# Performance work log

Hardware: AMD Instinct MI355X
Metric: run time of the kernel (lower is better)

Reference implementation:

```python
import jax, jax.numpy as jnp
import numpy as np

N_NODES = 100000
N_EDGES = 600000
IN_CH = 128
HID = 128


def setup_inputs() -> dict:
    key = jax.random.key(0)
    ks = jax.random.split(key, 8)
    x = jax.random.normal(ks[0], (N_NODES, IN_CH), dtype=jnp.float32)
    edge_index = jax.random.randint(ks[1], (2, N_EDGES), 0, N_NODES, dtype=jnp.int64)
    # Linear weights stored as (in, out); scaled like torch default init
    W1 = jax.random.normal(ks[2], (2 * IN_CH, HID), dtype=jnp.float32) / np.sqrt(2 * IN_CH)
    b1 = jnp.zeros((HID,), dtype=jnp.float32)
    W2 = jax.random.normal(ks[3], (HID, HID), dtype=jnp.float32) / np.sqrt(HID)
    b2 = jnp.zeros((HID,), dtype=jnp.float32)
    W3 = jax.random.normal(ks[4], (HID, 1), dtype=jnp.float32) / np.sqrt(HID)
    b3 = jnp.zeros((1,), dtype=jnp.float32)
    return {"x": x, "edge_index": edge_index, "W1": W1, "b1": b1,
            "W2": W2, "b2": b2, "W3": W3, "b3": b3}


def reference(x, edge_index, W1, b1, W2, b2, W3, b3):
    src = edge_index[0]
    tgt = edge_index[1]
    # gather + concat: [n_edges, 2*in_channels]
    h = jnp.concatenate([x[src, :], x[tgt, :]], axis=1)
    h = jax.nn.elu(h @ W1 + b1)
    h = jax.nn.elu(h @ W2 + b2)
    h = h @ W3 + b3  # [n_edges, 1]
    return jnp.squeeze(h)  # squeeze=True path -> [n_edges]
```

## Files before the change

kernel.cpp:

```cpp
#include <hip/hip_runtime.h>

#define N_NODES 100000
#define N_EDGES 600000
#define NT1 782
#define NT2 9375
#define LDH 136
#define G1H 512

typedef _Float16 f16x8 __attribute__((ext_vector_type(8)));
typedef __attribute__((ext_vector_type(4))) float f32x4;

__device__ __forceinline__ float elu_f(float v) {
    return v > 0.0f ? v : (__expf(v) - 1.0f);
}

extern "C" __global__ __launch_bounds__(256, 4)
void k1_node_linear(const float* __restrict__ x, const float* __restrict__ W1,
                    _Float16* __restrict__ P) {
    __shared__ __align__(16) _Float16 sX[128 * LDH];

    const int t = threadIdx.x;
    const int w = t >> 6, lane = t & 63;
    const int ln = lane & 15, kg = lane >> 4;
    const int kcf = t & 15;
    const int lef = t >> 4;
    const int half = (blockIdx.x >= G1H) ? 1 : 0;
    const int t0 = blockIdx.x - half * G1H;

    f16x8 bf[2][4];
#pragma unroll
    for (int c = 0; c < 2; ++c) {
        const int n = w * 32 + c * 16 + ln;
#pragma unroll
        for (int ks = 0; ks < 4; ++ks) {
            f16x8 v;
#pragma unroll
            for (int j = 0; j < 8; ++j) {
                int k = half * 128 + ks * 32 + kg * 8 + j;
                v[j] = (_Float16)W1[k * 128 + n];
            }
            bf[c][ks] = v;
        }
    }

    for (int tile = t0; tile < NT1; tile += G1H) {
        const int n0 = tile * 128;
        __syncthreads();
#pragma unroll 2
        for (int r = 0; r < 8; ++r) {
            int le = r * 16 + lef;
            int n = n0 + le;
            float4 a0 = make_float4(0.f, 0.f, 0.f, 0.f), a1 = a0;
            if (n < N_NODES) {
                const float* p = x + (size_t)n * 128 + kcf * 8;
                a0 = *(const float4*)p; a1 = *(const float4*)(p + 4);
            }
            float f[8] = {a0.x, a0.y, a0.z, a0.w, a1.x, a1.y, a1.z, a1.w};
            f16x8 vh;
#pragma unroll
            for (int j = 0; j < 8; ++j) vh[j] = (_Float16)f[j];
            *(f16x8*)(&sX[le * LDH + kcf * 8]) = vh;
        }
        __syncthreads();

        f32x4 acc[8][2];
#pragma unroll
        for (int rt = 0; rt < 8; ++rt)
#pragma unroll
            for (int c = 0; c < 2; ++c) acc[rt][c] = (f32x4){0.f, 0.f, 0.f, 0.f};

#pragma unroll
        for (int ks = 0; ks < 4; ++ks) {
#pragma unroll
            for (int rt = 0; rt < 8; ++rt) {
                f16x8 a = *(const f16x8*)(&sX[(rt * 16 + ln) * LDH + ks * 32 + kg * 8]);
#pragma unroll
                for (int c = 0; c < 2; ++c)
                    acc[rt][c] = __builtin_amdgcn_mfma_f32_16x16x32_f16(a, bf[c][ks], acc[rt][c], 0, 0, 0);
            }
        }

        __syncthreads();
#pragma unroll
        for (int rt = 0; rt < 8; ++rt)
#pragma unroll
            for (int c = 0; c < 2; ++c) {
                int col = w * 32 + c * 16 + ln;
#pragma unroll
                for (int reg = 0; reg < 4; ++reg) {
                    int row = rt * 16 + kg * 4 + reg;
                    sX[row * LDH + col] = (_Float16)acc[rt][c][reg];
                }
            }
        __syncthreads();
        {
            int row_l = t >> 1, seg = t & 1;
            int n = n0 + row_l;
            if (n < N_NODES) {
                _Float16* dst = P + (size_t)n * 256 + half * 128 + seg * 64;
                const _Float16* srcp = &sX[row_l * LDH + seg * 64];
#pragma unroll
                for (int i = 0; i < 8; ++i)
                    *(f16x8*)(dst + i * 8) = *(const f16x8*)(srcp + i * 8);
            }
        }
    }
}

extern "C" __global__ __launch_bounds__(256, 3)
void k2_edge_mlp(const _Float16* __restrict__ P, const void* __restrict__ eiv,
                 const float* __restrict__ b1, const float* __restrict__ W2,
                 const float* __restrict__ b2, const float* __restrict__ W3,
                 const float* __restrict__ b3, float* __restrict__ out) {
    __shared__ __align__(16) _Float16 sH[2][64 * LDH];
    __shared__ float sPart[2][4][64];
    __shared__ int sFlag;

    const int t = threadIdx.x;
    const int w = t >> 6, lane = t & 63;
    const int ln = lane & 15, kg = lane >> 4;
    const int row = t >> 2;
    const int kc0 = (t & 3) * 4;
    const float b3v = b3[0];
    const int stride = gridDim.x;

    if (t < 64) {
        unsigned v = ((const unsigned*)eiv)[2 * t + 1];
        unsigned long long bm = __ballot(v == 0u);
        if (t == 0) sFlag = (bm == ~0ull) ? 1 : 0;
    }

    f16x8 b1f[4];
#pragma unroll
    for (int i = 0; i < 4; ++i)
#pragma unroll
        for (int j = 0; j < 8; ++j) b1f[i][j] = (_Float16)b1[(kc0 + i) * 8 + j];

    float w3v[2], b2v[2];
#pragma unroll
    for (int c = 0; c < 2; ++c) {
        int col = w * 32 + c * 16 + ln;
        w3v[c] = W3[col]; b2v[c] = b2[col];
    }

    f16x8 bfw[2][4];
#pragma unroll
    for (int c = 0; c < 2; ++c) {
        const int n = w * 32 + c * 16 + ln;
#pragma unroll
        for (int ks = 0; ks < 4; ++ks) {
            f16x8 v;
#pragma unroll
            for (int j = 0; j < 8; ++j) {
                int k = ks * 32 + kg * 8 + j;
                v[j] = (_Float16)W2[k * 128 + n];
            }
            bfw[c][ks] = v;
        }
    }
    __syncthreads();
    const int mode64 = sFlag;

    const int tile0 = blockIdx.x;

    int se_nx, ge_nx;
    {
        int e = tile0 * 64 + row;
        if (mode64) {
            se_nx = (int)((const long long*)eiv)[e];
            ge_nx = (int)((const long long*)eiv)[N_EDGES + e];
        } else {
            se_nx = ((const int*)eiv)[e];
            ge_nx = ((const int*)eiv)[N_EDGES + e];
        }
    }
    {
        const _Float16* pa = P + (size_t)se_nx * 256 + kc0 * 8;
        const _Float16* pb = P + (size_t)ge_nx * 256 + 128 + kc0 * 8;
        f16x8 Ga[4], Gb[4];
#pragma unroll
        for (int i = 0; i < 4; ++i) {
            Ga[i] = *(const f16x8*)(pa + i * 8);
            Gb[i] = *(const f16x8*)(pb + i * 8);
        }
#pragma unroll
        for (int i = 0; i < 4; ++i) {
            f16x8 vh;
#pragma unroll
            for (int j = 0; j < 8; ++j)
                vh[j] = (_Float16)elu_f((float)Ga[i][j] + (float)Gb[i][j] + (float)b1f[i][j]);
            *(f16x8*)(&sH[0][row * LDH + (kc0 + i) * 8]) = vh;
        }
    }
    {
        int t1 = tile0 + stride;
        int t1c = (t1 < NT2) ? t1 : tile0;
        int e = t1c * 64 + row;
        if (mode64) {
            se_nx = (int)((const long long*)eiv)[e];
            ge_nx = (int)((const long long*)eiv)[N_EDGES + e];
        } else {
            se_nx = ((const int*)eiv)[e];
            ge_nx = ((const int*)eiv)[N_EDGES + e];
        }
    }
    __syncthreads();

    int p = 0;
    int prevE0 = -1;
    for (int tile = tile0; tile < NT2; tile += stride) {
        const int nt = tile + stride;
        const int ntc = (nt < NT2) ? nt : tile;

        const _Float16* pa = P + (size_t)se_nx * 256 + kc0 * 8;
        const _Float16* pb = P + (size_t)ge_nx * 256 + 128 + kc0 * 8;
        f16x8 Ga[4], Gb[4];
#pragma unroll
        for (int i = 0; i < 4; ++i) {
            Ga[i] = *(const f16x8*)(pa + i * 8);
            Gb[i] = *(const f16x8*)(pb + i * 8);
        }

        {
            int n2 = nt + stride;
            int n2c = (n2 < NT2) ? n2 : ntc;
            int e = n2c * 64 + row;
            if (mode64) {
                se_nx = (int)((const long long*)eiv)[e];
                ge_nx = (int)((const long long*)eiv)[N_EDGES + e];
            } else {
                se_nx = ((const int*)eiv)[e];
                ge_nx = ((const int*)eiv)[N_EDGES + e];
            }
        }

        if (prevE0 >= 0 && t < 64)
            out[prevE0 + t] = sPart[p ^ 1][0][t] + sPart[p ^ 1][1][t] +
                              sPart[p ^ 1][2][t] + sPart[p ^ 1][3][t] + b3v;

        f32x4 acc[4][2];
#pragma unroll
        for (int rt = 0; rt < 4; ++rt)
#pragma unroll
            for (int c = 0; c < 2; ++c) acc[rt][c] = (f32x4){0.f, 0.f, 0.f, 0.f};

#pragma unroll
        for (int ks = 0; ks < 4; ++ks) {
#pragma unroll
            for (int rt = 0; rt < 4; ++rt) {
                f16x8 a = *(const f16x8*)(&sH[p][(rt * 16 + ln) * LDH + ks * 32 + kg * 8]);
#pragma unroll
                for (int c = 0; c < 2; ++c)
                    acc[rt][c] = __builtin_amdgcn_mfma_f32_16x16x32_f16(a, bfw[c][ks], acc[rt][c], 0, 0, 0);
            }
        }

#pragma unroll
        for (int rt = 0; rt < 4; ++rt) {
            float pr[4] = {0.f, 0.f, 0.f, 0.f};
#pragma unroll
            for (int c = 0; c < 2; ++c) {
#pragma unroll
                for (int reg = 0; reg < 4; ++reg)
                    pr[reg] += elu_f(acc[rt][c][reg] + b2v[c]) * w3v[c];
            }
#pragma unroll
            for (int m = 1; m < 16; m <<= 1)
#pragma unroll
                for (int reg = 0; reg < 4; ++reg) pr[reg] += __shfl_xor(pr[reg], m, 64);
            if (ln == 0) {
#pragma unroll
                for (int reg = 0; reg < 4; ++reg)
                    sPart[p][w][rt * 16 + kg * 4 + reg] = pr[reg];
            }
        }

#pragma unroll
        for (int i = 0; i < 4; ++i) {
            f16x8 vh;
#pragma unroll
            for (int j = 0; j < 8; ++j)
                vh[j] = (_Float16)elu_f((float)Ga[i][j] + (float)Gb[i][j] + (float)b1f[i][j]);
            *(f16x8*)(&sH[p ^ 1][row * LDH + (kc0 + i) * 8]) = vh;
        }

        prevE0 = tile * 64;
        __syncthreads();
        p ^= 1;
    }

    if (prevE0 >= 0 && t < 64)
        out[prevE0 + t] = sPart[p ^ 1][0][t] + sPart[p ^ 1][1][t] +
                          sPart[p ^ 1][2][t] + sPart[p ^ 1][3][t] + b3v;
}

extern "C" void kernel_launch(void* const* d_in, const int* in_sizes, int n_in,
                              void* d_out, int out_size, void* d_ws, size_t ws_size,
                              hipStream_t stream) {
    const float* x  = (const float*)d_in[0];
    const void*  ei = d_in[1];
    const float* W1 = (const float*)d_in[2];
    const float* b1 = (const float*)d_in[3];
    const float* W2 = (const float*)d_in[4];
    const float* b2 = (const float*)d_in[5];
    const float* W3 = (const float*)d_in[6];
    const float* b3 = (const float*)d_in[7];
    float* out = (float*)d_out;

    _Float16* P = (_Float16*)((char*)d_ws + 256);

    k1_node_linear<<<1024, 256, 0, stream>>>(x, W1, P);
    k2_edge_mlp<<<768, 256, 0, stream>>>(P, ei, b1, W2, b2, W3, b3, out);
}
```

Before: 212.1 us.

## Compute both W1 halves per node tile in k1, one 64-node tile per block

The node-linear kernel now has each block load a 64-node tile of x once and multiply it by both halves of W1 (src and tgt projections). Before, the two halves ran in separate block groups that each re-read x, with a grid-stride loop over 128-node tiles. The intent is to halve x global reads and remove the loop, at the cost of twice the register-resident B fragments and more registers (launch bounds lowered to 3). The edge MLP kernel's occupancy hint and grid size are also raised, from 3 to 4 and from 768 to 1024 blocks.

```diff
diff --git a/kernel.cpp b/kernel.cpp
--- a/kernel.cpp
+++ b/kernel.cpp
@@ -2,11 +2,9 @@
 
 #define N_NODES 100000
 #define N_EDGES 600000
-#define NT1 782
+#define NT1B 1563
 #define NT2 9375
 #define LDH 136
-#define G1H 512
-
 typedef _Float16 f16x8 __attribute__((ext_vector_type(8)));
 typedef __attribute__((ext_vector_type(4))) float f32x4;
 
@@ -14,100 +12,105 @@
     return v > 0.0f ? v : (__expf(v) - 1.0f);
 }
 
-extern "C" __global__ __launch_bounds__(256, 4)
+extern "C" __global__ __launch_bounds__(256, 3)
 void k1_node_linear(const float* __restrict__ x, const float* __restrict__ W1,
                     _Float16* __restrict__ P) {
-    __shared__ __align__(16) _Float16 sX[128 * LDH];
+    __shared__ __align__(16) _Float16 sX[64 * LDH];
 
     const int t = threadIdx.x;
     const int w = t >> 6, lane = t & 63;
     const int ln = lane & 15, kg = lane >> 4;
-    const int kcf = t & 15;
-    const int lef = t >> 4;
-    const int half = (blockIdx.x >= G1H) ? 1 : 0;
-    const int t0 = blockIdx.x - half * G1H;
-
-    f16x8 bf[2][4];
-#pragma unroll
-    for (int c = 0; c < 2; ++c) {
-        const int n = w * 32 + c * 16 + ln;
-#pragma unroll
-        for (int ks = 0; ks < 4; ++ks) {
-            f16x8 v;
-#pragma unroll
-            for (int j = 0; j < 8; ++j) {
-                int k = half * 128 + ks * 32 + kg * 8 + j;
-                v[j] = (_Float16)W1[k * 128 + n];
-            }
-            bf[c][ks] = v;
-        }
-    }
-
-    for (int tile = t0; tile < NT1; tile += G1H) {
-        const int n0 = tile * 128;
-        __syncthreads();
-#pragma unroll 2
-        for (int r = 0; r < 8; ++r) {
-            int le = r * 16 + lef;
-            int n = n0 + le;
+    const int le = t >> 2;
+    const int q  = t & 3;
+
+    f16x8 bf[2][2][4];
+#pragma unroll
+    for (int half = 0; half < 2; ++half)
+#pragma unroll
+        for (int c = 0; c < 2; ++c) {
+            const int n = w * 32 + c * 16 + ln;
+#pragma unroll
+            for (int ks = 0; ks < 4; ++ks) {
+                f16x8 v;
+#pragma unroll
+                for (int j = 0; j < 8; ++j) {
+                    int k = half * 128 + ks * 32 + kg * 8 + j;
+                    v[j] = (_Float16)W1[k * 128 + n];
+                }
+                bf[half][c][ks] = v;
+            }
+        }
+
+    const int n0 = blockIdx.x * 64;
+
+    {
+        int n = n0 + le;
+#pragma unroll
+        for (int i = 0; i < 4; ++i) {
             float4 a0 = make_float4(0.f, 0.f, 0.f, 0.f), a1 = a0;
             if (n < N_NODES) {
-                const float* p = x + (size_t)n * 128 + kcf * 8;
+                const float* p = x + (size_t)n * 128 + q * 32 + i * 8;
                 a0 = *(const float4*)p; a1 = *(const float4*)(p + 4);
             }
-            float f[8] = {a0.x, a0.y, a0.z, a0.w, a1.x, a1.y, a1.z, a1.w};
             f16x8 vh;
-#pragma unroll
-            for (int j = 0; j < 8; ++j) vh[j] = (_Float16)f[j];
-            *(f16x8*)(&sX[le * LDH + kcf * 8]) = vh;
-        }
+            vh[0] = (_Float16)a0.x; vh[1] = (_Float16)a0.y;
+            vh[2] = (_Float16)a0.z; vh[3] = (_Float16)a0.w;
+            vh[4] = (_Float16)a1.x; vh[5] = (_Float16)a1.y;
+            vh[6] = (_Float16)a1.z; vh[7] = (_Float16)a1.w;
+            *(f16x8*)(&sX[le * LDH + q * 32 + i * 8]) = vh;
+        }
+    }
+    __syncthreads();
+
+    f32x4 acc[2][4][2];
+#pragma unroll
+    for (int half = 0; half < 2; ++half)
+#pragma unroll
+        for (int rt = 0; rt < 4; ++rt)
+#pragma unroll
+            for (int c = 0; c < 2; ++c) acc[half][rt][c] = (f32x4){0.f, 0.f, 0.f, 0.f};
+
+#pragma unroll
+    for (int ks = 0; ks < 4; ++ks) {
+#pragma unroll
+        for (int rt = 0; rt < 4; ++rt) {
+            f16x8 a = *(const f16x8*)(&sX[(rt * 16 + ln) * LDH + ks * 32 + kg * 8]);
+#pragma unroll
+            for (int half = 0; half < 2; ++half)
+#pragma unroll
+                for (int c = 0; c < 2; ++c)
+                    acc[half][rt][c] = __builtin_amdgcn_mfma_f32_16x16x32_f16(
+                        a, bf[half][c][ks], acc[half][rt][c], 0, 0, 0);
+        }
+    }
+
+#pragma unroll
+    for (int half = 0; half < 2; ++half) {
         __syncthreads();
-
-        f32x4 acc[8][2];
-#pragma unroll
-        for (int rt = 0; rt < 8; ++rt)
-#pragma unroll
-            for (int c = 0; c < 2; ++c) acc[rt][c] = (f32x4){0.f, 0.f, 0.f, 0.f};
-
-#pragma unroll
-        for (int ks = 0; ks < 4; ++ks) {
-#pragma unroll
-            for (int rt = 0; rt < 8; ++rt) {
-                f16x8 a = *(const f16x8*)(&sX[(rt * 16 + ln) * LDH + ks * 32 + kg * 8]);
-#pragma unroll
-                for (int c = 0; c < 2; ++c)
-                    acc[rt][c] = __builtin_amdgcn_mfma_f32_16x16x32_f16(a, bf[c][ks], acc[rt][c], 0, 0, 0);
-            }
-        }
-
-        __syncthreads();
-#pragma unroll
-        for (int rt = 0; rt < 8; ++rt)
+#pragma unroll
+        for (int rt = 0; rt < 4; ++rt)
 #pragma unroll
             for (int c = 0; c < 2; ++c) {
                 int col = w * 32 + c * 16 + ln;
 #pragma unroll
                 for (int reg = 0; reg < 4; ++reg) {
                     int row = rt * 16 + kg * 4 + reg;
-                    sX[row * LDH + col] = (_Float16)acc[rt][c][reg];
+                    sX[row * LDH + col] = (_Float16)acc[half][rt][c][reg];
                 }
             }
         __syncthreads();
-        {
-            int row_l = t >> 1, seg = t & 1;
-            int n = n0 + row_l;
-            if (n < N_NODES) {
-                _Float16* dst = P + (size_t)n * 256 + half * 128 + seg * 64;
-                const _Float16* srcp = &sX[row_l * LDH + seg * 64];
-#pragma unroll
-                for (int i = 0; i < 8; ++i)
-                    *(f16x8*)(dst + i * 8) = *(const f16x8*)(srcp + i * 8);
-            }
+        int n = n0 + le;
+        if (n < N_NODES) {
+            _Float16* dst = P + (size_t)n * 256 + half * 128 + q * 32;
+            const _Float16* srcp = &sX[le * LDH + q * 32];
+#pragma unroll
+            for (int i = 0; i < 4; ++i)
+                *(f16x8*)(dst + i * 8) = *(const f16x8*)(srcp + i * 8);
         }
     }
 }
 
-extern "C" __global__ __launch_bounds__(256, 3)
+extern "C" __global__ __launch_bounds__(256, 4)
 void k2_edge_mlp(const _Float16* __restrict__ P, const void* __restrict__ eiv,
                  const float* __restrict__ b1, const float* __restrict__ W2,
                  const float* __restrict__ b2, const float* __restrict__ W3,
@@ -309,6 +312,6 @@
 
     _Float16* P = (_Float16*)((char*)d_ws + 256);
 
-    k1_node_linear<<<1024, 256, 0, stream>>>(x, W1, P);
-    k2_edge_mlp<<<768, 256, 0, stream>>>(P, ei, b1, W2, b2, W3, b3, out);
+    k1_node_linear<<<NT1B, 256, 0, stream>>>(x, W1, P);
+    k2_edge_mlp<<<1024, 256, 0, stream>>>(P, ei, b1, W2, b2, W3, b3, out);
 }
```

After: 267.1 us. +25.9%, slower.
